# Optimization experiments

Hardware: AMD Instinct MI355X
Metric: run time of the kernel (lower is better)

Reference implementation:

```python
import jax, jax.numpy as jnp
import numpy as np

S, NB, C = 7, 2, 20
LAMBDA_COORD, LAMBDA_NOOBJ = 5.0, 0.5
EPS = 1e-6


def _iou(a, b):
    """Midpoint-format IoU. a, b: [..., 4] = (x, y, w, h)."""
    ax1, ay1 = a[..., 0] - a[..., 2] / 2, a[..., 1] - a[..., 3] / 2
    ax2, ay2 = a[..., 0] + a[..., 2] / 2, a[..., 1] + a[..., 3] / 2
    bx1, by1 = b[..., 0] - b[..., 2] / 2, b[..., 1] - b[..., 3] / 2
    bx2, by2 = b[..., 0] + b[..., 2] / 2, b[..., 1] + b[..., 3] / 2
    iw = jnp.clip(jnp.minimum(ax2, bx2) - jnp.maximum(ax1, bx1), 0.0)
    ih = jnp.clip(jnp.minimum(ay2, by2) - jnp.maximum(ay1, by1), 0.0)
    inter = iw * ih
    area_a = jnp.abs((ax2 - ax1) * (ay2 - ay1))
    area_b = jnp.abs((bx2 - bx1) * (by2 - by1))
    return inter / (area_a + area_b - inter + EPS)


def setup_inputs() -> dict:
    key = jax.random.key(0)
    k1, k2, k3, k4 = jax.random.split(key, 4)
    N = 16384
    predictions = jax.random.uniform(k1, (N, S * S * (C + NB * 5)), dtype=jnp.float32)
    cls = jax.random.uniform(k2, (N, S, S, C), dtype=jnp.float32)
    box_rest = jax.random.uniform(k3, (N, S, S, 4), dtype=jnp.float32)  # y,w,h,conf
    u = jax.random.uniform(k4, (N, S, S, 2), dtype=jnp.float32)
    flag = jnp.where(u[..., 0] < 0.3, 1.0, u[..., 1] * 0.99)
    targets = jnp.concatenate([cls, flag[..., None], box_rest], axis=-1)  # [N,S,S,25]
    return {"predictions": predictions, "targets": targets}


def reference(predictions, targets):
    N = predictions.shape[0]
    pred = predictions.reshape(N, S, S, C + NB * 5)
    class_pred = pred[..., :C]                      # [N,S,S,20]
    b1 = pred[..., C:C + 5]                         # [N,S,S,5]
    b2 = pred[..., C + 5:C + 10]                    # [N,S,S,5]
    tbox = targets[..., C:C + 5]                    # [N,S,S,5]
    obj = (targets[..., C] == 1.0).astype(pred.dtype)  # [N,S,S]

    iou1 = _iou(b1[..., :4], tbox[..., :4])
    iou2 = _iou(b2[..., :4], tbox[..., :4])
    resp = jnp.where((iou1 > iou2)[..., None], b1, b2)  # responsible box [N,S,S,5]

    xy = (resp[..., 0] - tbox[..., 0]) ** 2 + (resp[..., 1] - tbox[..., 1]) ** 2
    wh = (jnp.sqrt(resp[..., 2]) - jnp.sqrt(tbox[..., 2])) ** 2 \
       + (jnp.sqrt(resp[..., 3]) - jnp.sqrt(tbox[..., 3])) ** 2
    coord = LAMBDA_COORD * (xy + wh)
    conf = (resp[..., 4] - tbox[..., 4]) ** 2
    cls_loss = jnp.sum((class_pred - targets[..., :C]) ** 2, axis=-1)

    obj_terms = jnp.sum(obj * (coord + conf + cls_loss))
    noobj_terms = LAMBDA_NOOBJ * jnp.sum((1.0 - obj) * (b1[..., 4] ** 2 + b2[..., 4] ** 2))
    return (obj_terms + noobj_terms) / N
```

## Files before the change

### kernel.cpp

```cpp
#include <hip/hip_runtime.h>
#include <math.h>

#define SS 7
#define CC 20
#define CELL_PRED 30
#define CELL_TGT  25
#define BLOCK 256
#define GRID 1024

__device__ __forceinline__ float cell_loss(const float* __restrict__ pred,
                                           const float* __restrict__ tgt,
                                           int c) {
    const float EPS = 1e-6f;
    const float* tp = tgt + (size_t)c * CELL_TGT;
    float tv[CELL_TGT];
    #pragma unroll
    for (int j = 0; j < CELL_TGT; ++j) tv[j] = tp[j];

    const float2* p2 = (const float2*)(pred + (size_t)c * CELL_PRED);
    float cls = 0.0f;
    #pragma unroll
    for (int j = 0; j < 10; ++j) {
        float2 v = p2[j];
        float d0 = v.x - tv[2 * j];
        float d1 = v.y - tv[2 * j + 1];
        cls += d0 * d0;
        cls += d1 * d1;
    }
    float b[10];
    #pragma unroll
    for (int j = 0; j < 5; ++j) {
        float2 v = p2[10 + j];
        b[2 * j] = v.x; b[2 * j + 1] = v.y;
    }
    const float* b1 = b;
    const float* b2 = b + 5;
    const float* tb = tv + CC;

    float obj = (tb[0] == 1.0f) ? 1.0f : 0.0f;

    float t_x1 = tb[0] - tb[2] * 0.5f, t_y1 = tb[1] - tb[3] * 0.5f;
    float t_x2 = tb[0] + tb[2] * 0.5f, t_y2 = tb[1] + tb[3] * 0.5f;
    float t_area = fabsf((t_x2 - t_x1) * (t_y2 - t_y1));

    float a_x1 = b1[0] - b1[2] * 0.5f, a_y1 = b1[1] - b1[3] * 0.5f;
    float a_x2 = b1[0] + b1[2] * 0.5f, a_y2 = b1[1] + b1[3] * 0.5f;
    float iw1 = fmaxf(fminf(a_x2, t_x2) - fmaxf(a_x1, t_x1), 0.0f);
    float ih1 = fmaxf(fminf(a_y2, t_y2) - fmaxf(a_y1, t_y1), 0.0f);
    float inter1 = iw1 * ih1;
    float area1 = fabsf((a_x2 - a_x1) * (a_y2 - a_y1));
    float iou1 = inter1 / (area1 + t_area - inter1 + EPS);

    float c_x1 = b2[0] - b2[2] * 0.5f, c_y1 = b2[1] - b2[3] * 0.5f;
    float c_x2 = b2[0] + b2[2] * 0.5f, c_y2 = b2[1] + b2[3] * 0.5f;
    float iw2 = fmaxf(fminf(c_x2, t_x2) - fmaxf(c_x1, t_x1), 0.0f);
    float ih2 = fmaxf(fminf(c_y2, t_y2) - fmaxf(c_y1, t_y1), 0.0f);
    float inter2 = iw2 * ih2;
    float area2 = fabsf((c_x2 - c_x1) * (c_y2 - c_y1));
    float iou2 = inter2 / (area2 + t_area - inter2 + EPS);

    bool pick1 = iou1 > iou2;
    float r0 = pick1 ? b1[0] : b2[0];
    float r1 = pick1 ? b1[1] : b2[1];
    float r2 = pick1 ? b1[2] : b2[2];
    float r3 = pick1 ? b1[3] : b2[3];
    float r4 = pick1 ? b1[4] : b2[4];

    float dx = r0 - tb[0], dy = r1 - tb[1];
    float xy = dx * dx + dy * dy;
    float dw = sqrtf(r2) - sqrtf(tb[2]);
    float dh = sqrtf(r3) - sqrtf(tb[3]);
    float wh = dw * dw + dh * dh;
    float coord = 5.0f * (xy + wh);
    float dconf = r4 - tb[4];
    float conf = dconf * dconf;

    float noobj = 0.5f * (1.0f - obj) * (b1[4] * b1[4] + b2[4] * b2[4]);
    return obj * (coord + conf + cls) + noobj;
}

__global__ __launch_bounds__(BLOCK) void yolo_stream(
    const float* __restrict__ pred,
    const float* __restrict__ tgt,
    float* __restrict__ partials,
    int nCells, int fullIters)
{
    const int tid = threadIdx.x;
    int c = blockIdx.x * BLOCK + tid;
    const int stride = GRID * BLOCK;

    float loss = 0.0f;
    for (int it = 0; it < fullIters; ++it, c += stride)
        loss += cell_loss(pred, tgt, c);
    if (c < nCells)
        loss += cell_loss(pred, tgt, c);

    #pragma unroll
    for (int off = 32; off > 0; off >>= 1)
        loss += __shfl_down(loss, off, 64);
    __shared__ float s_red[4];
    if ((tid & 63) == 0) s_red[tid >> 6] = loss;
    __syncthreads();
    if (tid == 0)
        partials[blockIdx.x] = (s_red[0] + s_red[1]) + (s_red[2] + s_red[3]);
}

__global__ __launch_bounds__(BLOCK) void yolo_final_reduce(
    const float* __restrict__ partials, int nPartials, double invN,
    float* __restrict__ out)
{
    __shared__ double s_red[4];
    const float4* p4 = (const float4*)partials;
    double sum = 0.0;
    for (int i = threadIdx.x; i < (nPartials >> 2); i += BLOCK) {
        float4 v = p4[i];
        sum += (double)v.x + (double)v.y + (double)v.z + (double)v.w;
    }
    for (int i = ((nPartials >> 2) << 2) + threadIdx.x; i < nPartials; i += BLOCK)
        sum += (double)partials[i];
    #pragma unroll
    for (int off = 32; off > 0; off >>= 1)
        sum += __shfl_down(sum, off, 64);
    if ((threadIdx.x & 63) == 0) s_red[threadIdx.x >> 6] = sum;
    __syncthreads();
    if (threadIdx.x == 0) {
        double s = (s_red[0] + s_red[1]) + (s_red[2] + s_red[3]);
        out[0] = (float)(s * invN);
    }
}

extern "C" void kernel_launch(void* const* d_in, const int* in_sizes, int n_in,
                              void* d_out, int out_size, void* d_ws, size_t ws_size,
                              hipStream_t stream) {
    const float* pred = (const float*)d_in[0];
    const float* tgt  = (const float*)d_in[1];
    float* out = (float*)d_out;
    float* partials = (float*)d_ws;

    const int N = in_sizes[0] / (SS * SS * CELL_PRED);
    const int nCells = N * SS * SS;
    const int stride = GRID * BLOCK;
    const int fullIters = nCells / stride;

    yolo_stream<<<GRID, BLOCK, 0, stream>>>(pred, tgt, partials, nCells, fullIters);
    yolo_final_reduce<<<1, BLOCK, 0, stream>>>(partials, GRID, 1.0 / (double)N, out);
}
```

Baseline: 198.3 us.

## Process four cells per thread with 16-byte vector loads

Each thread now handles a group of four consecutive cells, so the group's prediction (120 floats) and target (100 floats) data are 16-byte aligned and can be read with float4 loads instead of float2 and scalar loads. The persistent grid-stride loop is replaced by a one-shot grid sized to the number of cell groups, and launch bounds request 3 blocks per CU. The aim is fewer, wider memory transactions for this bandwidth-bound loss. In exchange, per-thread accesses are strided by 480/400 bytes so coalescing across lanes is poor, register pressure rises, and any trailing cells beyond a multiple of four are dropped (the test size divides evenly).

```diff
diff --git a/kernel.cpp b/kernel.cpp
--- a/kernel.cpp
+++ b/kernel.cpp
@@ -6,94 +6,96 @@
 #define CELL_PRED 30
 #define CELL_TGT  25
 #define BLOCK 256
-#define GRID 1024
 
-__device__ __forceinline__ float cell_loss(const float* __restrict__ pred,
-                                           const float* __restrict__ tgt,
-                                           int c) {
-    const float EPS = 1e-6f;
-    const float* tp = tgt + (size_t)c * CELL_TGT;
-    float tv[CELL_TGT];
-    #pragma unroll
-    for (int j = 0; j < CELL_TGT; ++j) tv[j] = tp[j];
-
-    const float2* p2 = (const float2*)(pred + (size_t)c * CELL_PRED);
-    float cls = 0.0f;
-    #pragma unroll
-    for (int j = 0; j < 10; ++j) {
-        float2 v = p2[j];
-        float d0 = v.x - tv[2 * j];
-        float d1 = v.y - tv[2 * j + 1];
-        cls += d0 * d0;
-        cls += d1 * d1;
-    }
-    float b[10];
-    #pragma unroll
-    for (int j = 0; j < 5; ++j) {
-        float2 v = p2[10 + j];
-        b[2 * j] = v.x; b[2 * j + 1] = v.y;
-    }
-    const float* b1 = b;
-    const float* b2 = b + 5;
-    const float* tb = tv + CC;
-
-    float obj = (tb[0] == 1.0f) ? 1.0f : 0.0f;
-
-    float t_x1 = tb[0] - tb[2] * 0.5f, t_y1 = tb[1] - tb[3] * 0.5f;
-    float t_x2 = tb[0] + tb[2] * 0.5f, t_y2 = tb[1] + tb[3] * 0.5f;
-    float t_area = fabsf((t_x2 - t_x1) * (t_y2 - t_y1));
-
-    float a_x1 = b1[0] - b1[2] * 0.5f, a_y1 = b1[1] - b1[3] * 0.5f;
-    float a_x2 = b1[0] + b1[2] * 0.5f, a_y2 = b1[1] + b1[3] * 0.5f;
-    float iw1 = fmaxf(fminf(a_x2, t_x2) - fmaxf(a_x1, t_x1), 0.0f);
-    float ih1 = fmaxf(fminf(a_y2, t_y2) - fmaxf(a_y1, t_y1), 0.0f);
-    float inter1 = iw1 * ih1;
-    float area1 = fabsf((a_x2 - a_x1) * (a_y2 - a_y1));
-    float iou1 = inter1 / (area1 + t_area - inter1 + EPS);
-
-    float c_x1 = b2[0] - b2[2] * 0.5f, c_y1 = b2[1] - b2[3] * 0.5f;
-    float c_x2 = b2[0] + b2[2] * 0.5f, c_y2 = b2[1] + b2[3] * 0.5f;
-    float iw2 = fmaxf(fminf(c_x2, t_x2) - fmaxf(c_x1, t_x1), 0.0f);
-    float ih2 = fmaxf(fminf(c_y2, t_y2) - fmaxf(c_y1, t_y1), 0.0f);
-    float inter2 = iw2 * ih2;
-    float area2 = fabsf((c_x2 - c_x1) * (c_y2 - c_y1));
-    float iou2 = inter2 / (area2 + t_area - inter2 + EPS);
-
-    bool pick1 = iou1 > iou2;
-    float r0 = pick1 ? b1[0] : b2[0];
-    float r1 = pick1 ? b1[1] : b2[1];
-    float r2 = pick1 ? b1[2] : b2[2];
-    float r3 = pick1 ? b1[3] : b2[3];
-    float r4 = pick1 ? b1[4] : b2[4];
-
-    float dx = r0 - tb[0], dy = r1 - tb[1];
-    float xy = dx * dx + dy * dy;
-    float dw = sqrtf(r2) - sqrtf(tb[2]);
-    float dh = sqrtf(r3) - sqrtf(tb[3]);
-    float wh = dw * dw + dh * dh;
-    float coord = 5.0f * (xy + wh);
-    float dconf = r4 - tb[4];
-    float conf = dconf * dconf;
-
-    float noobj = 0.5f * (1.0f - obj) * (b1[4] * b1[4] + b2[4] * b2[4]);
-    return obj * (coord + conf + cls) + noobj;
-}
-
-__global__ __launch_bounds__(BLOCK) void yolo_stream(
+__global__ __launch_bounds__(BLOCK, 3) void yolo_stream4(
     const float* __restrict__ pred,
     const float* __restrict__ tgt,
     float* __restrict__ partials,
-    int nCells, int fullIters)
+    int nQuads)
 {
+    const float EPS = 1e-6f;
     const int tid = threadIdx.x;
-    int c = blockIdx.x * BLOCK + tid;
-    const int stride = GRID * BLOCK;
+    const int q = blockIdx.x * BLOCK + tid;
 
     float loss = 0.0f;
-    for (int it = 0; it < fullIters; ++it, c += stride)
-        loss += cell_loss(pred, tgt, c);
-    if (c < nCells)
-        loss += cell_loss(pred, tgt, c);
+    if (q < nQuads) {
+        const float4* p4 = (const float4*)pred + (size_t)q * (CELL_PRED);
+        const float4* t4 = (const float4*)tgt  + (size_t)q * (CELL_TGT);
+
+        #pragma unroll
+        for (int k = 0; k < 4; ++k) {
+            const int pf = (30 * k) >> 2, po = (30 * k) & 3;
+            const int tf = (25 * k) >> 2, to = (25 * k) & 3;
+
+            float pw[32], tw[28];
+            #pragma unroll
+            for (int j = 0; j < 8; ++j) {
+                float4 v = p4[pf + j];
+                pw[4 * j] = v.x; pw[4 * j + 1] = v.y;
+                pw[4 * j + 2] = v.z; pw[4 * j + 3] = v.w;
+            }
+            #pragma unroll
+            for (int j = 0; j < 7; ++j) {
+                float4 v = t4[tf + j];
+                tw[4 * j] = v.x; tw[4 * j + 1] = v.y;
+                tw[4 * j + 2] = v.z; tw[4 * j + 3] = v.w;
+            }
+            const float* p = pw + po;
+            const float* t = tw + to;
+
+            const float* b1 = p + CC;
+            const float* b2 = p + CC + 5;
+            const float* tb = t + CC;
+
+            float obj = (tb[0] == 1.0f) ? 1.0f : 0.0f;
+
+            float t_x1 = tb[0] - tb[2] * 0.5f, t_y1 = tb[1] - tb[3] * 0.5f;
+            float t_x2 = tb[0] + tb[2] * 0.5f, t_y2 = tb[1] + tb[3] * 0.5f;
+            float t_area = fabsf((t_x2 - t_x1) * (t_y2 - t_y1));
+
+            float a_x1 = b1[0] - b1[2] * 0.5f, a_y1 = b1[1] - b1[3] * 0.5f;
+            float a_x2 = b1[0] + b1[2] * 0.5f, a_y2 = b1[1] + b1[3] * 0.5f;
+            float iw1 = fmaxf(fminf(a_x2, t_x2) - fmaxf(a_x1, t_x1), 0.0f);
+            float ih1 = fmaxf(fminf(a_y2, t_y2) - fmaxf(a_y1, t_y1), 0.0f);
+            float inter1 = iw1 * ih1;
+            float area1 = fabsf((a_x2 - a_x1) * (a_y2 - a_y1));
+            float iou1 = inter1 / (area1 + t_area - inter1 + EPS);
+
+            float c_x1 = b2[0] - b2[2] * 0.5f, c_y1 = b2[1] - b2[3] * 0.5f;
+            float c_x2 = b2[0] + b2[2] * 0.5f, c_y2 = b2[1] + b2[3] * 0.5f;
+            float iw2 = fmaxf(fminf(c_x2, t_x2) - fmaxf(c_x1, t_x1), 0.0f);
+            float ih2 = fmaxf(fminf(c_y2, t_y2) - fmaxf(c_y1, t_y1), 0.0f);
+            float inter2 = iw2 * ih2;
+            float area2 = fabsf((c_x2 - c_x1) * (c_y2 - c_y1));
+            float iou2 = inter2 / (area2 + t_area - inter2 + EPS);
+
+            bool pick1 = iou1 > iou2;
+            float r0 = pick1 ? b1[0] : b2[0];
+            float r1 = pick1 ? b1[1] : b2[1];
+            float r2 = pick1 ? b1[2] : b2[2];
+            float r3 = pick1 ? b1[3] : b2[3];
+            float r4 = pick1 ? b1[4] : b2[4];
+
+            float dx = r0 - tb[0], dy = r1 - tb[1];
+            float xy = dx * dx + dy * dy;
+            float dw = sqrtf(r2) - sqrtf(tb[2]);
+            float dh = sqrtf(r3) - sqrtf(tb[3]);
+            float wh = dw * dw + dh * dh;
+            float coord = 5.0f * (xy + wh);
+            float dconf = r4 - tb[4];
+            float conf = dconf * dconf;
+
+            float cls = 0.0f;
+            #pragma unroll
+            for (int kk = 0; kk < CC; ++kk) {
+                float d = p[kk] - t[kk];
+                cls += d * d;
+            }
+
+            float noobj = 0.5f * (1.0f - obj) * (b1[4] * b1[4] + b2[4] * b2[4]);
+            loss += obj * (coord + conf + cls) + noobj;
+        }
+    }
 
     #pragma unroll
     for (int off = 32; off > 0; off >>= 1)
@@ -139,9 +141,9 @@
 
     const int N = in_sizes[0] / (SS * SS * CELL_PRED);
     const int nCells = N * SS * SS;
-    const int stride = GRID * BLOCK;
-    const int fullIters = nCells / stride;
+    const int nQuads = nCells / 4;
+    const int grid = (nQuads + BLOCK - 1) / BLOCK;
 
-    yolo_stream<<<GRID, BLOCK, 0, stream>>>(pred, tgt, partials, nCells, fullIters);
-    yolo_final_reduce<<<1, BLOCK, 0, stream>>>(partials, GRID, 1.0 / (double)N, out);
+    yolo_stream4<<<grid, BLOCK, 0, stream>>>(pred, tgt, partials, nQuads);
+    yolo_final_reduce<<<1, BLOCK, 0, stream>>>(partials, grid, 1.0 / (double)N, out);
 }
```

Result: slower. 265.6 us (+33.9%).
